# Kernel tuning notes

Hardware: AMD Instinct MI355X
Metric: run time of the kernel (lower is better)

Reference implementation:

```python
import jax, jax.numpy as jnp
import numpy as np

VOCAB, EMB, HID = 5000, 512, 1024


def setup_inputs() -> dict:
    key = jax.random.key(0)
    ks = jax.random.split(key, 8)
    s = lambda k, shape, fan: jax.random.normal(k, shape, jnp.float32) * (1.0 / np.sqrt(fan))
    return {
        "x": jax.random.randint(ks[0], (32, 512), 0, VOCAB, dtype=jnp.int32),
        "emb": jax.random.normal(ks[1], (VOCAB, EMB), jnp.float32),
        "W_ih": s(ks[2], (4 * HID, EMB), HID),   # PyTorch gate order: i, f, g, o
        "W_hh": s(ks[3], (4 * HID, HID), HID),
        "b_ih": s(ks[4], (4 * HID,), HID),
        "b_hh": s(ks[5], (4 * HID,), HID),
        "W_fc": s(ks[6], (VOCAB, HID), HID),
        "b_fc": s(ks[7], (VOCAB,), HID),
    }


def _lstm(xe, W_ih, W_hh, b_ih, b_hh):
    B, S, E = xe.shape
    H = W_hh.shape[1]
    # Precompute input contributions for all timesteps: [B,S,4H]
    xg = jnp.einsum('bse,ge->bsg', xe, W_ih) + b_ih + b_hh
    xg = jnp.swapaxes(xg, 0, 1)  # [S,B,4H]

    def step(carry, xg_t):
        h, c = carry
        gates = xg_t + h @ W_hh.T  # [B,4H]
        i, f, g, o = jnp.split(gates, 4, axis=-1)
        i, f, o = jax.nn.sigmoid(i), jax.nn.sigmoid(f), jax.nn.sigmoid(o)
        g = jnp.tanh(g)
        c = f * c + i * g
        h = o * jnp.tanh(c)
        return (h, c), h

    h0 = jnp.zeros((B, H), xe.dtype)
    c0 = jnp.zeros((B, H), xe.dtype)
    (hT, cT), hs = jax.lax.scan(step, (h0, c0), xg)
    return jnp.swapaxes(hs, 0, 1), (hT, cT)  # [B,S,H]


def reference(x, emb, W_ih, W_hh, b_ih, b_hh, W_fc, b_fc):
    xe = emb[x]  # [B,S,E] embedding lookup
    out, _state = _lstm(xe, W_ih, W_hh, b_ih, b_hh)
    logits = jnp.einsum('bsh,vh->bsv', out, W_fc) + b_fc  # [B,S,V]
    return logits
```

## Files before the change

### kernel.cpp

```cpp
#include <hip/hip_runtime.h>
#include <hip/hip_bf16.h>

using bf16x8 = __attribute__((ext_vector_type(8))) __bf16;
using f32x4  = __attribute__((ext_vector_type(4))) float;

constexpr int NB = 32;
constexpr int NS = 512;
constexpr int NE = 512;
constexpr int NH = 1024;
constexpr int NV = 5000;
constexpr int NG = 4096;

constexpr int LSTM_BLOCKS = 64;

__device__ __forceinline__ float blo(unsigned u) {
    union { unsigned i; float f; } v; v.i = u << 16; return v.f;
}
__device__ __forceinline__ unsigned short f2bf(float f) {
    union { float f; unsigned i; } v; v.f = f;
    unsigned r = v.i + 0x7fffu + ((v.i >> 16) & 1u);
    return (unsigned short)(r >> 16);
}
__device__ __forceinline__ uint4 pack8(float4 a, float4 b) {
    uint4 r;
    r.x = (unsigned)f2bf(a.x) | ((unsigned)f2bf(a.y) << 16);
    r.y = (unsigned)f2bf(a.z) | ((unsigned)f2bf(a.w) << 16);
    r.z = (unsigned)f2bf(b.x) | ((unsigned)f2bf(b.y) << 16);
    r.w = (unsigned)f2bf(b.z) | ((unsigned)f2bf(b.w) << 16);
    return r;
}

__device__ __forceinline__ uint4 load_b128_llc(const void* p) {
    uint4 r;
    asm volatile("global_load_dwordx4 %0, %1, off sc0 sc1" : "=v"(r) : "v"(p));
    return r;
}
__device__ __forceinline__ void store_short_llc(void* p, unsigned v) {
    asm volatile("global_store_short %0, %1, off sc0 sc1" :: "v"(p), "v"(v) : "memory");
}
__device__ __forceinline__ void wait_vm0() {
    asm volatile("s_waitcnt vmcnt(0)" ::: "memory");
}

__global__ __launch_bounds__(256) void k_embed_gemm(
    const int* __restrict__ x,
    const float* __restrict__ emb,
    const float* __restrict__ W_ih,
    const float* __restrict__ b_ih,
    const float* __restrict__ b_hh,
    unsigned short* __restrict__ xgT)
{
    constexpr int BK = 32, LDP = BK + 8;
    __shared__ __align__(16) unsigned short Ash[64 * LDP];
    __shared__ __align__(16) unsigned short Bsh[64 * LDP];
    __shared__ int ids[64];

    const int tid = threadIdx.x;
    const int m0 = blockIdx.y * 64;
    const int n0 = blockIdx.x * 64;
    if (tid < 64) ids[tid] = x[m0 + tid];
    __syncthreads();

    const int wave = tid >> 6, lane = tid & 63;
    const int wm = (wave >> 1) * 32, wn = (wave & 1) * 32;
    const int fr = lane & 15, kq = lane >> 4;

    const int sr = tid >> 2;
    const int sc = (tid & 3) * 8;

    f32x4 acc[2][2] = {};

    for (int k0 = 0; k0 < NE; k0 += BK) {
        const float* ap = emb + (size_t)ids[sr] * NE + k0 + sc;
        const float* bp = W_ih + (size_t)(n0 + sr) * NE + k0 + sc;
        float4 af0 = *(const float4*)ap, af1 = *(const float4*)(ap + 4);
        float4 bf0 = *(const float4*)bp, bf1 = *(const float4*)(bp + 4);
        *(uint4*)(Ash + sr * LDP + sc) = pack8(af0, af1);
        *(uint4*)(Bsh + sr * LDP + sc) = pack8(bf0, bf1);
        __syncthreads();
        bf16x8 a0 = *(const bf16x8*)(Ash + (wm + fr) * LDP + kq * 8);
        bf16x8 a1 = *(const bf16x8*)(Ash + (wm + 16 + fr) * LDP + kq * 8);
        bf16x8 b0 = *(const bf16x8*)(Bsh + (wn + fr) * LDP + kq * 8);
        bf16x8 b1 = *(const bf16x8*)(Bsh + (wn + 16 + fr) * LDP + kq * 8);
        acc[0][0] = __builtin_amdgcn_mfma_f32_16x16x32_bf16(a0, b0, acc[0][0], 0, 0, 0);
        acc[0][1] = __builtin_amdgcn_mfma_f32_16x16x32_bf16(a0, b1, acc[0][1], 0, 0, 0);
        acc[1][0] = __builtin_amdgcn_mfma_f32_16x16x32_bf16(a1, b0, acc[1][0], 0, 0, 0);
        acc[1][1] = __builtin_amdgcn_mfma_f32_16x16x32_bf16(a1, b1, acc[1][1], 0, 0, 0);
        __syncthreads();
    }

    for (int i = 0; i < 2; ++i)
        for (int j = 0; j < 2; ++j) {
            const int row = m0 + wm + i * 16 + kq * 4;
            const int col = n0 + wn + j * 16 + fr;
            const int g = col >> 10, jblk = (col >> 4) & 63, u = col & 15;
            const float bias = b_ih[col] + b_hh[col];
            for (int r = 0; r < 4; ++r) {
                const int m = row + r, b = m >> 9, s = m & 511;
                xgT[((((size_t)s * 4 + g) * 64 + jblk) * 32 + b) * 16 + u] =
                    f2bf(acc[i][j][r] + bias);
            }
        }
}

__global__ __launch_bounds__(256, 1) void k_lstm_persist(
    const unsigned short* __restrict__ xgT,
    const float* __restrict__ W_hh,
    unsigned short* __restrict__ hs,
    unsigned* __restrict__ bar)
{
    __shared__ __align__(16) unsigned short h_sh[32 * 1024];
    __shared__ float gates_sh[32 * 65];
    __shared__ float c_sh[32 * 17];

    const int tid  = threadIdx.x;
    const int wave = tid >> 6, lane = tid & 63;
    const int fr = lane & 15, kq = lane >> 4;
    const int bid = blockIdx.x;
    const int j0 = bid * 16;

    bf16x8 bfrag[32];
    {
        const float* wrow = W_hh + (size_t)(wave * NH + j0 + fr) * NH;
#pragma unroll
        for (int ks = 0; ks < 32; ++ks) {
            const float* wp = wrow + ks * 32 + kq * 8;
            float4 w0 = *(const float4*)wp, w1 = *(const float4*)(wp + 4);
            uint4 pk = pack8(w0, w1);
            bfrag[ks] = *(bf16x8*)&pk;
        }
    }

    {
        uint4 z = {0, 0, 0, 0};
#pragma unroll
        for (int r = 0; r < 16; ++r)
            *(uint4*)((char*)h_sh + r * 4096 + tid * 16) = z;
        for (int i = tid; i < 32 * 17; i += 256) c_sh[i] = 0.f;
    }
    __syncthreads();

    const int srow = tid >> 7;
    const int sc16 = tid & 127;
    const int swz  = (fr & 7) << 4;
    const int au = tid & 15;
    const int ab = tid >> 4;

    for (int t = 0; t < NS; ++t) {
        unsigned short xv[2][4];
#pragma unroll
        for (int p = 0; p < 2; ++p) {
            const int b = ab + p * 16;
            const unsigned short* xp =
                xgT + ((((size_t)t * 4) * 64 + bid) * 32 + b) * 16 + au;
#pragma unroll
            for (int g = 0; g < 4; ++g) xv[p][g] = xp[(size_t)g * (64 * 32 * 16)];
        }

        if (t > 0) {
            uint4 stg[16];
#pragma unroll
            for (int r = 0; r < 16; ++r) {
                const int b = r * 2 + srow;
                stg[r] = load_b128_llc(hs + ((size_t)b * NS + (t - 1)) * NH + sc16 * 8);
            }
            wait_vm0();
            __builtin_amdgcn_sched_barrier(0);
#pragma unroll
            for (int r = 0; r < 16; ++r) {
                const int b = r * 2 + srow;
                int off = b * 2048 + sc16 * 16;
                off ^= (b & 7) << 4;
                *(uint4*)((char*)h_sh + off) = stg[r];
            }
        }
        __syncthreads();

        f32x4 acc0 = {}, acc1 = {};
#pragma unroll
        for (int ks = 0; ks < 32; ++ks) {
            const int cb = ks * 64 + kq * 16;
            bf16x8 a0 = *(const bf16x8*)((const char*)h_sh + ((fr * 2048 + cb) ^ swz));
            bf16x8 a1 = *(const bf16x8*)((const char*)h_sh + (((fr + 16) * 2048 + cb) ^ swz));
            acc0 = __builtin_amdgcn_mfma_f32_16x16x32_bf16(a0, bfrag[ks], acc0, 0, 0, 0);
            acc1 = __builtin_amdgcn_mfma_f32_16x16x32_bf16(a1, bfrag[ks], acc1, 0, 0, 0);
        }

#pragma unroll
        for (int r = 0; r < 4; ++r) {
            gates_sh[(kq * 4 + r) * 65 + wave * 16 + fr]      = acc0[r];
            gates_sh[(16 + kq * 4 + r) * 65 + wave * 16 + fr] = acc1[r];
        }
        __syncthreads();

#pragma unroll
        for (int p = 0; p < 2; ++p) {
            const int b = ab + p * 16, u = au;
            const float gi = gates_sh[b * 65 +      u] + blo((unsigned)xv[p][0]);
            const float gf = gates_sh[b * 65 + 16 + u] + blo((unsigned)xv[p][1]);
            const float gg = gates_sh[b * 65 + 32 + u] + blo((unsigned)xv[p][2]);
            const float go = gates_sh[b * 65 + 48 + u] + blo((unsigned)xv[p][3]);
            const float ig = 1.f / (1.f + __expf(-gi));
            const float fg = 1.f / (1.f + __expf(-gf));
            const float g2 = tanhf(gg);
            const float og = 1.f / (1.f + __expf(-go));
            const float cn = fg * c_sh[b * 17 + u] + ig * g2;
            c_sh[b * 17 + u] = cn;
            const unsigned short hv = f2bf(og * tanhf(cn));
            store_short_llc(hs + ((size_t)b * NS + t) * NH + j0 + u, (unsigned)hv);
        }

        wait_vm0();
        __syncthreads();
        if (tid == 0) {
            unsigned a = __hip_atomic_fetch_add(&bar[0], 1u, __ATOMIC_RELAXED,
                                                __HIP_MEMORY_SCOPE_AGENT);
            if (a == (unsigned)(LSTM_BLOCKS * (t + 1) - 1)) {
                __hip_atomic_store(&bar[1], (unsigned)(t + 1), __ATOMIC_RELEASE,
                                   __HIP_MEMORY_SCOPE_AGENT);
            } else {
                int spins = 0;
                while (__hip_atomic_load(&bar[1], __ATOMIC_RELAXED,
                                         __HIP_MEMORY_SCOPE_AGENT) < (unsigned)(t + 1)) {
                    __builtin_amdgcn_s_sleep(2);
                    if (++spins > 100000) break;
                }
            }
        }
        __syncthreads();
        __builtin_amdgcn_sched_barrier(0);
    }
}

__global__ __launch_bounds__(256) void k_logits_gemm(
    const unsigned short* __restrict__ hs,
    const float* __restrict__ W_fc,
    const float* __restrict__ b_fc,
    float* __restrict__ out)
{
    constexpr int BK = 32, LDP = BK + 8;
    __shared__ __align__(16) unsigned short Ash[64 * LDP];
    __shared__ __align__(16) unsigned short Bsh[64 * LDP];

    const int tid = threadIdx.x;
    const int m0 = blockIdx.y * 64;
    const int n0 = blockIdx.x * 64;

    const int wave = tid >> 6, lane = tid & 63;
    const int wm = (wave >> 1) * 32, wn = (wave & 1) * 32;
    const int fr = lane & 15, kq = lane >> 4;

    const int sr = tid >> 2;
    const int sc = (tid & 3) * 8;
    const int brow = min(n0 + sr, NV - 1);

    f32x4 acc[2][2] = {};

    for (int k0 = 0; k0 < NH; k0 += BK) {
        const float* bp = W_fc + (size_t)brow * NH + k0 + sc;
        float4 bf0 = *(const float4*)bp, bf1 = *(const float4*)(bp + 4);
        *(uint4*)(Ash + sr * LDP + sc) =
            *(const uint4*)(hs + (size_t)(m0 + sr) * NH + k0 + sc);
        *(uint4*)(Bsh + sr * LDP + sc) = pack8(bf0, bf1);
        __syncthreads();
        bf16x8 a0 = *(const bf16x8*)(Ash + (wm + fr) * LDP + kq * 8);
        bf16x8 a1 = *(const bf16x8*)(Ash + (wm + 16 + fr) * LDP + kq * 8);
        bf16x8 b0 = *(const bf16x8*)(Bsh + (wn + fr) * LDP + kq * 8);
        bf16x8 b1 = *(const bf16x8*)(Bsh + (wn + 16 + fr) * LDP + kq * 8);
        acc[0][0] = __builtin_amdgcn_mfma_f32_16x16x32_bf16(a0, b0, acc[0][0], 0, 0, 0);
        acc[0][1] = __builtin_amdgcn_mfma_f32_16x16x32_bf16(a0, b1, acc[0][1], 0, 0, 0);
        acc[1][0] = __builtin_amdgcn_mfma_f32_16x16x32_bf16(a1, b0, acc[1][0], 0, 0, 0);
        acc[1][1] = __builtin_amdgcn_mfma_f32_16x16x32_bf16(a1, b1, acc[1][1], 0, 0, 0);
        __syncthreads();
    }

    for (int i = 0; i < 2; ++i)
        for (int j = 0; j < 2; ++j) {
            const int row = m0 + wm + i * 16 + kq * 4;
            const int col = n0 + wn + j * 16 + fr;
            if (col < NV) {
                const float bias = b_fc[col];
                for (int r = 0; r < 4; ++r)
                    out[(size_t)(row + r) * NV + col] = acc[i][j][r] + bias;
            }
        }
}

extern "C" void kernel_launch(void* const* d_in, const int* in_sizes, int n_in,
                              void* d_out, int out_size, void* d_ws, size_t ws_size,
                              hipStream_t stream)
{
    const int*   x    = (const int*)d_in[0];
    const float* emb  = (const float*)d_in[1];
    const float* W_ih = (const float*)d_in[2];
    const float* W_hh = (const float*)d_in[3];
    const float* b_ih = (const float*)d_in[4];
    const float* b_hh = (const float*)d_in[5];
    const float* W_fc = (const float*)d_in[6];
    const float* b_fc = (const float*)d_in[7];
    float*       out  = (float*)d_out;

    char* w = (char*)d_ws;
    const size_t XG_BYTES = (size_t)NB * NS * NG * 2;
    const size_t HS_BYTES = (size_t)NB * NS * NH * 2;
    unsigned short* xgT = (unsigned short*)w;
    unsigned short* hsb = (unsigned short*)(w + XG_BYTES);
    unsigned*       bar = (unsigned*)(w + XG_BYTES + HS_BYTES);

    hipMemsetAsync(bar, 0, 2 * sizeof(unsigned), stream);

    k_embed_gemm<<<dim3(NG / 64, (NB * NS) / 64), 256, 0, stream>>>(
        x, emb, W_ih, b_ih, b_hh, xgT);

    k_lstm_persist<<<dim3(LSTM_BLOCKS), 256, 0, stream>>>(xgT, W_hh, hsb, bar);

    k_logits_gemm<<<dim3((NV + 63) / 64, (NB * NS) / 64), 256, 0, stream>>>(
        hsb, W_fc, b_fc, out);
}
```

Measured before the change: 4.562 ms.

## Use per-block flags barrier, prefetch xg, pre-convert W_fc, enlarge logits tiles

Replaces the counter-based grid barrier in the persistent LSTM with per-block release flags that wave 0 polls together with a wave-wide vote. The next timestep's input gate values are now loaded before the wait, so that load latency overlaps the barrier. W_fc is converted to bf16 once in a separate kernel that reuses the dead xgT workspace region. The logits GEMM moves to 128x128 tiles with 4x4 MFMA accumulators per wave, which raises data reuse per tile. The spin loop no longer sleeps, which adds memory polling traffic, and it breaks out silently after a bounded number of spins.

```diff
diff --git a/kernel.cpp b/kernel.cpp
--- a/kernel.cpp
+++ b/kernel.cpp
@@ -107,7 +107,7 @@
     const unsigned short* __restrict__ xgT,
     const float* __restrict__ W_hh,
     unsigned short* __restrict__ hs,
-    unsigned* __restrict__ bar)
+    unsigned* __restrict__ flags)
 {
     __shared__ __align__(16) unsigned short h_sh[32 * 1024];
     __shared__ float gates_sh[32 * 65];
@@ -146,17 +146,16 @@
     const int au = tid & 15;
     const int ab = tid >> 4;
 
+    unsigned short xv[2][4], xn[2][4];
+#pragma unroll
+    for (int p = 0; p < 2; ++p) {
+        const int b = ab + p * 16;
+        const unsigned short* xp = xgT + (((size_t)0 * 4 * 64 + bid) * 32 + b) * 16 + au;
+#pragma unroll
+        for (int g = 0; g < 4; ++g) xv[p][g] = xp[(size_t)g * (64 * 32 * 16)];
+    }
+
     for (int t = 0; t < NS; ++t) {
-        unsigned short xv[2][4];
-#pragma unroll
-        for (int p = 0; p < 2; ++p) {
-            const int b = ab + p * 16;
-            const unsigned short* xp =
-                xgT + ((((size_t)t * 4) * 64 + bid) * 32 + b) * 16 + au;
-#pragma unroll
-            for (int g = 0; g < 4; ++g) xv[p][g] = xp[(size_t)g * (64 * 32 * 16)];
-        }
-
         if (t > 0) {
             uint4 stg[16];
 #pragma unroll
@@ -212,70 +211,100 @@
 
         wait_vm0();
         __syncthreads();
-        if (tid == 0) {
-            unsigned a = __hip_atomic_fetch_add(&bar[0], 1u, __ATOMIC_RELAXED,
-                                                __HIP_MEMORY_SCOPE_AGENT);
-            if (a == (unsigned)(LSTM_BLOCKS * (t + 1) - 1)) {
-                __hip_atomic_store(&bar[1], (unsigned)(t + 1), __ATOMIC_RELEASE,
-                                   __HIP_MEMORY_SCOPE_AGENT);
-            } else {
-                int spins = 0;
-                while (__hip_atomic_load(&bar[1], __ATOMIC_RELAXED,
-                                         __HIP_MEMORY_SCOPE_AGENT) < (unsigned)(t + 1)) {
-                    __builtin_amdgcn_s_sleep(2);
-                    if (++spins > 100000) break;
-                }
-            }
-        }
-        __syncthreads();
-        __builtin_amdgcn_sched_barrier(0);
-    }
+        if (tid == 0)
+            __hip_atomic_store(&flags[bid * 16], (unsigned)(t + 1),
+                               __ATOMIC_RELEASE, __HIP_MEMORY_SCOPE_AGENT);
+
+        {
+            const int tn = (t + 1 < NS) ? t + 1 : t;
+#pragma unroll
+            for (int p = 0; p < 2; ++p) {
+                const int b = ab + p * 16;
+                const unsigned short* xp =
+                    xgT + (((size_t)tn * 4 * 64 + bid) * 32 + b) * 16 + au;
+#pragma unroll
+                for (int g = 0; g < 4; ++g) xn[p][g] = xp[(size_t)g * (64 * 32 * 16)];
+            }
+        }
+
+        if (wave == 0) {
+            const unsigned tgt = (unsigned)(t + 1);
+            int spins = 0;
+            for (;;) {
+                unsigned f = __hip_atomic_load(&flags[lane * 16], __ATOMIC_RELAXED,
+                                               __HIP_MEMORY_SCOPE_AGENT);
+                if (__all(f >= tgt)) break;
+                if (++spins > (1 << 20)) break;
+            }
+        }
+        __syncthreads();
+
+#pragma unroll
+        for (int p = 0; p < 2; ++p)
+#pragma unroll
+            for (int g = 0; g < 4; ++g) xv[p][g] = xn[p][g];
+    }
+}
+
+__global__ __launch_bounds__(256) void k_convert_wfc(
+    const float* __restrict__ W_fc, unsigned short* __restrict__ W_fcb)
+{
+    const size_t i = ((size_t)blockIdx.x * 256 + threadIdx.x) * 8;
+    float4 a = *(const float4*)(W_fc + i);
+    float4 b = *(const float4*)(W_fc + i + 4);
+    *(uint4*)(W_fcb + i) = pack8(a, b);
 }
 
 __global__ __launch_bounds__(256) void k_logits_gemm(
     const unsigned short* __restrict__ hs,
-    const float* __restrict__ W_fc,
+    const unsigned short* __restrict__ W_fcb,
     const float* __restrict__ b_fc,
     float* __restrict__ out)
 {
     constexpr int BK = 32, LDP = BK + 8;
-    __shared__ __align__(16) unsigned short Ash[64 * LDP];
-    __shared__ __align__(16) unsigned short Bsh[64 * LDP];
+    __shared__ __align__(16) unsigned short Ash[128 * LDP];
+    __shared__ __align__(16) unsigned short Bsh[128 * LDP];
 
     const int tid = threadIdx.x;
-    const int m0 = blockIdx.y * 64;
-    const int n0 = blockIdx.x * 64;
+    const int m0 = blockIdx.y * 128;
+    const int n0 = blockIdx.x * 128;
 
     const int wave = tid >> 6, lane = tid & 63;
-    const int wm = (wave >> 1) * 32, wn = (wave & 1) * 32;
+    const int wm = (wave >> 1) * 64, wn = (wave & 1) * 64;
     const int fr = lane & 15, kq = lane >> 4;
 
-    const int sr = tid >> 2;
-    const int sc = (tid & 3) * 8;
+    const int sr = tid >> 1;
+    const int sc = (tid & 1) * 16;
     const int brow = min(n0 + sr, NV - 1);
 
-    f32x4 acc[2][2] = {};
+    f32x4 acc[4][4] = {};
 
     for (int k0 = 0; k0 < NH; k0 += BK) {
-        const float* bp = W_fc + (size_t)brow * NH + k0 + sc;
-        float4 bf0 = *(const float4*)bp, bf1 = *(const float4*)(bp + 4);
-        *(uint4*)(Ash + sr * LDP + sc) =
-            *(const uint4*)(hs + (size_t)(m0 + sr) * NH + k0 + sc);
-        *(uint4*)(Bsh + sr * LDP + sc) = pack8(bf0, bf1);
-        __syncthreads();
-        bf16x8 a0 = *(const bf16x8*)(Ash + (wm + fr) * LDP + kq * 8);
-        bf16x8 a1 = *(const bf16x8*)(Ash + (wm + 16 + fr) * LDP + kq * 8);
-        bf16x8 b0 = *(const bf16x8*)(Bsh + (wn + fr) * LDP + kq * 8);
-        bf16x8 b1 = *(const bf16x8*)(Bsh + (wn + 16 + fr) * LDP + kq * 8);
-        acc[0][0] = __builtin_amdgcn_mfma_f32_16x16x32_bf16(a0, b0, acc[0][0], 0, 0, 0);
-        acc[0][1] = __builtin_amdgcn_mfma_f32_16x16x32_bf16(a0, b1, acc[0][1], 0, 0, 0);
-        acc[1][0] = __builtin_amdgcn_mfma_f32_16x16x32_bf16(a1, b0, acc[1][0], 0, 0, 0);
-        acc[1][1] = __builtin_amdgcn_mfma_f32_16x16x32_bf16(a1, b1, acc[1][1], 0, 0, 0);
-        __syncthreads();
-    }
-
-    for (int i = 0; i < 2; ++i)
-        for (int j = 0; j < 2; ++j) {
+        const unsigned short* ap = hs + (size_t)(m0 + sr) * NH + k0 + sc;
+        const unsigned short* bp = W_fcb + (size_t)brow * NH + k0 + sc;
+        uint4 a0 = *(const uint4*)ap, a1 = *(const uint4*)(ap + 8);
+        uint4 b0 = *(const uint4*)bp, b1 = *(const uint4*)(bp + 8);
+        *(uint4*)(Ash + sr * LDP + sc)     = a0;
+        *(uint4*)(Ash + sr * LDP + sc + 8) = a1;
+        *(uint4*)(Bsh + sr * LDP + sc)     = b0;
+        *(uint4*)(Bsh + sr * LDP + sc + 8) = b1;
+        __syncthreads();
+        bf16x8 af[4], bf[4];
+#pragma unroll
+        for (int i = 0; i < 4; ++i) {
+            af[i] = *(const bf16x8*)(Ash + (wm + i * 16 + fr) * LDP + kq * 8);
+            bf[i] = *(const bf16x8*)(Bsh + (wn + i * 16 + fr) * LDP + kq * 8);
+        }
+#pragma unroll
+        for (int i = 0; i < 4; ++i)
+#pragma unroll
+            for (int j = 0; j < 4; ++j)
+                acc[i][j] = __builtin_amdgcn_mfma_f32_16x16x32_bf16(af[i], bf[j], acc[i][j], 0, 0, 0);
+        __syncthreads();
+    }
+
+    for (int i = 0; i < 4; ++i)
+        for (int j = 0; j < 4; ++j) {
             const int row = m0 + wm + i * 16 + kq * 4;
             const int col = n0 + wn + j * 16 + fr;
             if (col < NV) {
@@ -303,17 +332,20 @@
     char* w = (char*)d_ws;
     const size_t XG_BYTES = (size_t)NB * NS * NG * 2;
     const size_t HS_BYTES = (size_t)NB * NS * NH * 2;
-    unsigned short* xgT = (unsigned short*)w;
-    unsigned short* hsb = (unsigned short*)(w + XG_BYTES);
-    unsigned*       bar = (unsigned*)(w + XG_BYTES + HS_BYTES);
-
-    hipMemsetAsync(bar, 0, 2 * sizeof(unsigned), stream);
+    unsigned short* xgT   = (unsigned short*)w;
+    unsigned short* hsb   = (unsigned short*)(w + XG_BYTES);
+    unsigned*       flags = (unsigned*)(w + XG_BYTES + HS_BYTES);
+    unsigned short* W_fcb = (unsigned short*)w;
+
+    hipMemsetAsync(flags, 0, LSTM_BLOCKS * 64, stream);
 
     k_embed_gemm<<<dim3(NG / 64, (NB * NS) / 64), 256, 0, stream>>>(
         x, emb, W_ih, b_ih, b_hh, xgT);
 
-    k_lstm_persist<<<dim3(LSTM_BLOCKS), 256, 0, stream>>>(xgT, W_hh, hsb, bar);
-
-    k_logits_gemm<<<dim3((NV + 63) / 64, (NB * NS) / 64), 256, 0, stream>>>(
-        hsb, W_fc, b_fc, out);
-}
+    k_lstm_persist<<<dim3(LSTM_BLOCKS), 256, 0, stream>>>(xgT, W_hh, hsb, flags);
+
+    k_convert_wfc<<<dim3((NV * NH) / (256 * 8)), 256, 0, stream>>>(W_fc, W_fcb);
+
+    k_logits_gemm<<<dim3((NV + 127) / 128, (NB * NS) / 128), 256, 0, stream>>>(
+        hsb, W_fcb, b_fc, out);
+}
```

After: 4.016 ms. -12.0%, faster.
